# Optimization experiments

Hardware: AMD Instinct MI355X
Metric: run time of the kernel (lower is better)

Reference implementation:

```python
import jax, jax.numpy as jnp
import numpy as np

B, S, H, V = 32, 512, 1024, 250002


def setup_inputs() -> dict:
    key = jax.random.key(0)
    k1, k2, k3 = jax.random.split(key, 3)
    hidden_states = jax.random.normal(k1, (B, S, H), dtype=jnp.float32)
    input_ids = jax.random.randint(k2, (B, S), 0, V, dtype=jnp.int32)
    attention_mask = jnp.ones((B, S), dtype=jnp.float32)
    W = jax.random.normal(k3, (1, H), dtype=jnp.float32) * (1.0 / np.sqrt(H))
    b = jnp.zeros((1,), dtype=jnp.float32)
    return {"hidden_states": hidden_states, "input_ids": input_ids,
            "attention_mask": attention_mask, "W": W, "b": b}


def reference(hidden_states, input_ids, attention_mask, W, b):
    # linear(hidden,1).squeeze(-1): [B,S]
    token_weights = jnp.einsum('bsh,h->bs', hidden_states, W[0]) + b[0]
    token_weights = token_weights * attention_mask
    token_weights = jax.nn.relu(token_weights)
    # scatter-add each token weight into its vocab bin, per batch row.
    # Flatten (batch, token_id) -> single segment id so one segment_sum handles all rows.
    flat_ids = (input_ids + V * jnp.arange(B, dtype=input_ids.dtype)[:, None]).reshape(-1)
    sparse_embedding = jax.ops.segment_sum(
        token_weights.reshape(-1), flat_ids, num_segments=B * V)
    return sparse_embedding.reshape(B, V)
```

## Files before the change

kernel.cpp:

```cpp
#include <hip/hip_runtime.h>
#include <hip/hip_bf16.h>

#define BB 32
#define SS 512
#define HH 1024
#define VV 250002
#define TOKENS (BB * SS)
#define OUT_FLOATS (BB * VV)
#define OUT_F4 (OUT_FLOATS / 4)

typedef float floatx4 __attribute__((ext_vector_type(4)));

#define Z_BLOCKS 2048
#define Z_THREADS 256
__global__ __launch_bounds__(Z_THREADS) void k1_zero(float* __restrict__ out)
{
    const int tid = blockIdx.x * Z_THREADS + threadIdx.x;
    floatx4* __restrict__ o4 = reinterpret_cast<floatx4*>(out);
    const floatx4 z = {0.f, 0.f, 0.f, 0.f};
    for (int i = tid; i < OUT_F4; i += Z_BLOCKS * Z_THREADS)
        __builtin_nontemporal_store(z, &o4[i]);
}

#define D_BLOCKS 2048
#define D_THREADS 256
__global__ __launch_bounds__(D_THREADS) void k2_dot_scatter(
    const float* __restrict__ hidden,
    const int* __restrict__ ids,
    const float* __restrict__ mask,
    const float* __restrict__ W,
    const float* __restrict__ bias,
    float* __restrict__ out)
{
    const int tid = blockIdx.x * D_THREADS + threadIdx.x;
    const int lane = threadIdx.x & 63;
    const int wave = tid >> 6;

    const float4* __restrict__ w4 = reinterpret_cast<const float4*>(W);
    const float bias0 = bias[0];

    const float4* __restrict__ h4a =
        reinterpret_cast<const float4*>(hidden + (size_t)(wave * 2 + 0) * HH);
    const float4* __restrict__ h4b =
        reinterpret_cast<const float4*>(hidden + (size_t)(wave * 2 + 1) * HH);

    float4 ha[4], hb[4], wv[4];
#pragma unroll
    for (int i = 0; i < 4; ++i) ha[i] = h4a[i * 64 + lane];
#pragma unroll
    for (int i = 0; i < 4; ++i) hb[i] = h4b[i * 64 + lane];
#pragma unroll
    for (int i = 0; i < 4; ++i) wv[i] = w4[i * 64 + lane];

    float sa = 0.f, sb = 0.f;
#pragma unroll
    for (int i = 0; i < 4; ++i) {
        sa = fmaf(ha[i].x, wv[i].x, sa); sa = fmaf(ha[i].y, wv[i].y, sa);
        sa = fmaf(ha[i].z, wv[i].z, sa); sa = fmaf(ha[i].w, wv[i].w, sa);
        sb = fmaf(hb[i].x, wv[i].x, sb); sb = fmaf(hb[i].y, wv[i].y, sb);
        sb = fmaf(hb[i].z, wv[i].z, sb); sb = fmaf(hb[i].w, wv[i].w, sb);
    }

#pragma unroll
    for (int off = 32; off > 0; off >>= 1) {
        sa += __shfl_xor(sa, off, 64);
        sb += __shfl_xor(sb, off, 64);
    }

    if (lane == 0) {
        const int t0 = wave * 2;
        const float twa = fmaxf((sa + bias0) * mask[t0], 0.0f);
        const float twb = fmaxf((sb + bias0) * mask[t0 + 1], 0.0f);
        if (twa != 0.0f)
            atomicAdd(&out[(size_t)(t0 / SS) * VV + ids[t0]], twa);
        if (twb != 0.0f)
            atomicAdd(&out[(size_t)((t0 + 1) / SS) * VV + ids[t0 + 1]], twb);
    }
}

extern "C" void kernel_launch(void* const* d_in, const int* in_sizes, int n_in,
                              void* d_out, int out_size, void* d_ws, size_t ws_size,
                              hipStream_t stream) {
    const float* hidden = (const float*)d_in[0];
    const int*   ids    = (const int*)d_in[1];
    const float* mask   = (const float*)d_in[2];
    const float* W      = (const float*)d_in[3];
    const float* bias   = (const float*)d_in[4];
    float* out = (float*)d_out;

    k1_zero<<<Z_BLOCKS, Z_THREADS, 0, stream>>>(out);
    k2_dot_scatter<<<D_BLOCKS, D_THREADS, 0, stream>>>(hidden, ids, mask, W, bias, out);
}
```

Baseline: 23.61 us.

## Fuse output zeroing with dot product, defer scatter to a second kernel

Output zeroing is merged into the dot-product kernel so the zero stores overlap with the hidden-state loads. The computed token weights go to a workspace buffer, and a small second kernel does the atomic scatter into the output. The zero stores also switch from nontemporal to regular stores. The cost is an extra workspace round trip and one more small kernel, but the ordering between zeroing and the atomics still holds across the kernel boundary.

```diff
diff --git a/kernel.cpp b/kernel.cpp
--- a/kernel.cpp
+++ b/kernel.cpp
@@ -9,36 +9,23 @@
 #define OUT_FLOATS (BB * VV)
 #define OUT_F4 (OUT_FLOATS / 4)
 
-typedef float floatx4 __attribute__((ext_vector_type(4)));
+#define K1_BLOCKS 2048
+#define K1_THREADS 256
+#define K1_TID (K1_BLOCKS * K1_THREADS)
 
-#define Z_BLOCKS 2048
-#define Z_THREADS 256
-__global__ __launch_bounds__(Z_THREADS) void k1_zero(float* __restrict__ out)
-{
-    const int tid = blockIdx.x * Z_THREADS + threadIdx.x;
-    floatx4* __restrict__ o4 = reinterpret_cast<floatx4*>(out);
-    const floatx4 z = {0.f, 0.f, 0.f, 0.f};
-    for (int i = tid; i < OUT_F4; i += Z_BLOCKS * Z_THREADS)
-        __builtin_nontemporal_store(z, &o4[i]);
-}
-
-#define D_BLOCKS 2048
-#define D_THREADS 256
-__global__ __launch_bounds__(D_THREADS) void k2_dot_scatter(
+__global__ __launch_bounds__(K1_THREADS) void k1_zero_and_dot(
     const float* __restrict__ hidden,
-    const int* __restrict__ ids,
     const float* __restrict__ mask,
     const float* __restrict__ W,
     const float* __restrict__ bias,
-    float* __restrict__ out)
+    float* __restrict__ out,
+    float* __restrict__ tw_ws)
 {
-    const int tid = blockIdx.x * D_THREADS + threadIdx.x;
+    const int tid = blockIdx.x * K1_THREADS + threadIdx.x;
     const int lane = threadIdx.x & 63;
     const int wave = tid >> 6;
 
     const float4* __restrict__ w4 = reinterpret_cast<const float4*>(W);
-    const float bias0 = bias[0];
-
     const float4* __restrict__ h4a =
         reinterpret_cast<const float4*>(hidden + (size_t)(wave * 2 + 0) * HH);
     const float4* __restrict__ h4b =
@@ -52,6 +39,11 @@
 #pragma unroll
     for (int i = 0; i < 4; ++i) wv[i] = w4[i * 64 + lane];
 
+    float4* __restrict__ o4 = reinterpret_cast<float4*>(out);
+    const float4 z = make_float4(0.f, 0.f, 0.f, 0.f);
+    for (int i = tid; i < OUT_F4; i += K1_TID)
+        o4[i] = z;
+
     float sa = 0.f, sb = 0.f;
 #pragma unroll
     for (int i = 0; i < 4; ++i) {
@@ -60,7 +52,6 @@
         sb = fmaf(hb[i].x, wv[i].x, sb); sb = fmaf(hb[i].y, wv[i].y, sb);
         sb = fmaf(hb[i].z, wv[i].z, sb); sb = fmaf(hb[i].w, wv[i].w, sb);
     }
-
 #pragma unroll
     for (int off = 32; off > 0; off >>= 1) {
         sa += __shfl_xor(sa, off, 64);
@@ -69,13 +60,22 @@
 
     if (lane == 0) {
         const int t0 = wave * 2;
-        const float twa = fmaxf((sa + bias0) * mask[t0], 0.0f);
-        const float twb = fmaxf((sb + bias0) * mask[t0 + 1], 0.0f);
-        if (twa != 0.0f)
-            atomicAdd(&out[(size_t)(t0 / SS) * VV + ids[t0]], twa);
-        if (twb != 0.0f)
-            atomicAdd(&out[(size_t)((t0 + 1) / SS) * VV + ids[t0 + 1]], twb);
+        const float bias0 = bias[0];
+        tw_ws[t0]     = fmaxf((sa + bias0) * mask[t0], 0.0f);
+        tw_ws[t0 + 1] = fmaxf((sb + bias0) * mask[t0 + 1], 0.0f);
     }
+}
+
+__global__ __launch_bounds__(256) void k2_scatter(
+    const float* __restrict__ tw_ws,
+    const int* __restrict__ ids,
+    float* __restrict__ out)
+{
+    const int t = blockIdx.x * 256 + threadIdx.x;
+    if (t >= TOKENS) return;
+    const float tw = tw_ws[t];
+    if (tw != 0.0f)
+        atomicAdd(&out[(size_t)(t / SS) * VV + ids[t]], tw);
 }
 
 extern "C" void kernel_launch(void* const* d_in, const int* in_sizes, int n_in,
@@ -86,8 +86,9 @@
     const float* mask   = (const float*)d_in[2];
     const float* W      = (const float*)d_in[3];
     const float* bias   = (const float*)d_in[4];
-    float* out = (float*)d_out;
+    float* out   = (float*)d_out;
+    float* tw_ws = (float*)d_ws;
 
-    k1_zero<<<Z_BLOCKS, Z_THREADS, 0, stream>>>(out);
-    k2_dot_scatter<<<D_BLOCKS, D_THREADS, 0, stream>>>(hidden, ids, mask, W, bias, out);
+    k1_zero_and_dot<<<K1_BLOCKS, K1_THREADS, 0, stream>>>(hidden, mask, W, bias, out, tw_ws);
+    k2_scatter<<<(TOKENS + 255) / 256, 256, 0, stream>>>(tw_ws, ids, out);
 }
```

New measurement: 21.76 us. -7.8%, faster.
